# Optimization experiments

Measured on AMD Instinct MI355X. Metric: run time of the kernel, lower is better.

The kernel has to match this reference:

```python
import jax, jax.numpy as jnp
import numpy as np

EPS = 1e-6
BASE_TAU = 1.0  # temperature, learnable_tau=False


def setup_inputs() -> dict:
    key = jax.random.key(0)
    k1, k2, k3 = jax.random.split(key, 3)
    n, b, t, h = 16, 4, 2048, 1024
    num_blocks = 24
    return {
        "values": jax.random.normal(k1, (n, b, t, h), dtype=jnp.float32),
        "w_query": jax.random.normal(k2, (num_blocks, h), dtype=jnp.float32) * 0.02,
        "key_pos_bias": jax.random.normal(k3, (num_blocks, h), dtype=jnp.float32) * 0.02,
        "position": 16,
    }


def reference(values, w_query, key_pos_bias, position):
    # values: [n, b, t, h] stacked completed block outputs, n == position
    fp = values.astype(jnp.float32)
    # weight-free RMSNorm (BlockAttnRes._rms_norm)
    inv = jax.lax.rsqrt(jnp.mean(fp * fp, axis=-1, keepdims=True) + EPS)
    keys = fp * inv
    # positional bias for the first `position` block slots
    keys = keys + key_pos_bias[:position].astype(keys.dtype)[:, None, None, :]
    query = w_query[position].astype(jnp.float32)  # [h]
    scale = jnp.sqrt(jnp.float32(values.shape[-1])) * BASE_TAU
    scores = jnp.einsum('h,nbth->nbt', query, keys) / scale  # [n, b, t]
    alpha = jax.nn.softmax(scores, axis=0)                    # softmax over history n
    routed = jnp.einsum('nbt,nbth->bth', alpha, fp).astype(values.dtype)
    alpha_bth = jnp.transpose(alpha, (1, 2, 0))               # [b, t, n]
    return routed, alpha_bth
```

## Files before the change

kernel.cpp:

```cpp
#include <hip/hip_runtime.h>
#include <math.h>

#define H     1024
#define NBLK  16
#define BT    8192
#define ROUTED_SIZE (BT * H)
#define SCALE_INV (1.0f / 32.0f)

typedef float v4f __attribute__((ext_vector_type(4)));

__global__ __launch_bounds__(1024) void qb_kernel(
    const float* __restrict__ w_query,
    const float* __restrict__ key_pos_bias,
    const int*   __restrict__ pos_p,
    float*       __restrict__ qb)
{
    const int n    = threadIdx.x >> 6;
    const int lane = threadIdx.x & 63;
    const int pos  = *pos_p;

    const float* q = w_query      + (size_t)pos * H;
    const float* b = key_pos_bias + (size_t)n   * H;

    float s = 0.0f;
#pragma unroll
    for (int j = 0; j < 4; ++j) {
        const int h = lane * 16 + j * 4;
        const float4 qv = *(const float4*)(q + h);
        const float4 bv = *(const float4*)(b + h);
        s += qv.x * bv.x + qv.y * bv.y + qv.z * bv.z + qv.w * bv.w;
    }
#pragma unroll
    for (int off = 32; off; off >>= 1) s += __shfl_xor(s, off, 64);
    if (lane == 0) qb[n] = s;
}

__global__ __launch_bounds__(256, 4) void block_attn_res_kernel(
    const float* __restrict__ values,
    const float* __restrict__ w_query,
    const int*   __restrict__ pos_p,
    const float* __restrict__ qb,
    float*       __restrict__ out)
{
    const int bt  = blockIdx.x;
    const int tid = threadIdx.x;
    const int h0  = tid << 2;

    const int pos = *pos_p;
    const v4f q = *(const v4f*)(w_query + (size_t)pos * H + h0);

    v4f v[NBLK];
    const float* vbase = values + (size_t)bt * H + h0;
#pragma unroll
    for (int n = 0; n < NBLK; ++n)
        v[n] = __builtin_nontemporal_load((const v4f*)(vbase + (size_t)n * BT * H));

    __shared__ float2 pv[NBLK][256];

#pragma unroll
    for (int n = 0; n < NBLK; ++n) {
        const v4f x  = v[n];
        const v4f xx = x * x;
        const v4f qx = q * x;
        const float ss = (xx[0] + xx[1]) + (xx[2] + xx[3]);
        const float qv = (qx[0] + qx[1]) + (qx[2] + qx[3]);
        pv[n][tid] = make_float2(ss, qv);
    }
    __syncthreads();

    {
        const int n2 = tid >> 4;
        const int c  = tid & 15;
        float ss = 0.0f, qv = 0.0f;
#pragma unroll
        for (int k = 0; k < 16; ++k) {
            const float2 p = pv[n2][k * 16 + c];
            ss += p.x; qv += p.y;
        }
#pragma unroll
        for (int off = 1; off <= 8; off <<= 1) {
            ss += __shfl_xor(ss, off, 64);
            qv += __shfl_xor(qv, off, 64);
        }
        if (c == 0) {
            const float inv = rsqrtf(ss * (1.0f / (float)H) + 1e-6f);
            pv[n2][0].x = (inv * qv + qb[n2]) * SCALE_INV;
        }
    }
    __syncthreads();

    float m = -3.402823466e38f;
#pragma unroll
    for (int n = 0; n < NBLK; ++n) m = fmaxf(m, pv[n][0].x);

    float a[NBLK];
    float sum = 0.0f;
#pragma unroll
    for (int n = 0; n < NBLK; ++n) { a[n] = __expf(pv[n][0].x - m); sum += a[n]; }
    const float rs = 1.0f / sum;

    v4f acc = {0.0f, 0.0f, 0.0f, 0.0f};
#pragma unroll
    for (int n = 0; n < NBLK; ++n) acc += (a[n] * rs) * v[n];
    __builtin_nontemporal_store(acc, (v4f*)(out + (size_t)bt * H + h0));

    if (tid < NBLK)
        out[(size_t)ROUTED_SIZE + (size_t)bt * NBLK + tid]
            = __expf(pv[tid][0].x - m) * rs;
}

extern "C" void kernel_launch(void* const* d_in, const int* in_sizes, int n_in,
                              void* d_out, int out_size, void* d_ws, size_t ws_size,
                              hipStream_t stream) {
    const float* values       = (const float*)d_in[0];
    const float* w_query      = (const float*)d_in[1];
    const float* key_pos_bias = (const float*)d_in[2];
    const int*   position     = (const int*)d_in[3];
    float*       out          = (float*)d_out;
    float*       qb           = (float*)d_ws;

    hipLaunchKernelGGL(qb_kernel, dim3(1), dim3(1024), 0, stream,
                       w_query, key_pos_bias, position, qb);
    hipLaunchKernelGGL(block_attn_res_kernel, dim3(BT), dim3(256), 0, stream,
                       values, w_query, position, qb, out);
}
```

Measured before the change: 674.0 us.

## Split history dimension across four thread groups per block with 1024 threads

Each block now uses 1024 threads, with four groups of 256 each loading four of the sixteen history slices. This replaces one 256-thread block holding all sixteen vec4 loads in registers, cutting registers per thread and raising memory-level parallelism. The weighted partial sums are reduced through shared memory, and the score reduction now uses full-wavefront shuffles. The loads also change from nontemporal to ordinary loads. In exchange the block gains an extra barrier and a shared-memory round trip, and the large blocks may limit occupancy.

```diff
diff --git a/kernel.cpp b/kernel.cpp
--- a/kernel.cpp
+++ b/kernel.cpp
@@ -35,7 +35,7 @@
     if (lane == 0) qb[n] = s;
 }
 
-__global__ __launch_bounds__(256, 4) void block_attn_res_kernel(
+__global__ __launch_bounds__(1024, 8) void block_attn_res_kernel(
     const float* __restrict__ values,
     const float* __restrict__ w_query,
     const int*   __restrict__ pos_p,
@@ -44,69 +44,82 @@
 {
     const int bt  = blockIdx.x;
     const int tid = threadIdx.x;
-    const int h0  = tid << 2;
+    const int c   = tid & 255;
+    const int g   = tid >> 8;
+    const int h0  = c << 2;
+
+    __shared__ float2 pv[NBLK][256];
+    __shared__ v4f    rp[4][256];
+    __shared__ float  scores[NBLK];
 
     const int pos = *pos_p;
     const v4f q = *(const v4f*)(w_query + (size_t)pos * H + h0);
 
-    v4f v[NBLK];
-    const float* vbase = values + (size_t)bt * H + h0;
+    v4f v[4];
+    const float* vbase = values + (size_t)bt * H + h0 + (size_t)g * 4 * BT * H;
 #pragma unroll
-    for (int n = 0; n < NBLK; ++n)
-        v[n] = __builtin_nontemporal_load((const v4f*)(vbase + (size_t)n * BT * H));
-
-    __shared__ float2 pv[NBLK][256];
+    for (int i = 0; i < 4; ++i)
+        v[i] = *(const v4f*)(vbase + (size_t)i * BT * H);
 
 #pragma unroll
-    for (int n = 0; n < NBLK; ++n) {
-        const v4f x  = v[n];
+    for (int i = 0; i < 4; ++i) {
+        const v4f x  = v[i];
         const v4f xx = x * x;
         const v4f qx = q * x;
-        const float ss = (xx[0] + xx[1]) + (xx[2] + xx[3]);
-        const float qv = (qx[0] + qx[1]) + (qx[2] + qx[3]);
-        pv[n][tid] = make_float2(ss, qv);
+        pv[g * 4 + i][c] = make_float2((xx[0] + xx[1]) + (xx[2] + xx[3]),
+                                       (qx[0] + qx[1]) + (qx[2] + qx[3]));
     }
     __syncthreads();
 
     {
-        const int n2 = tid >> 4;
-        const int c  = tid & 15;
-        float ss = 0.0f, qv = 0.0f;
+        const int n2   = tid >> 6;
+        const int lane = tid & 63;
+        const float2 p0 = pv[n2][lane];
+        const float2 p1 = pv[n2][lane + 64];
+        const float2 p2 = pv[n2][lane + 128];
+        const float2 p3 = pv[n2][lane + 192];
+        float ss = (p0.x + p1.x) + (p2.x + p3.x);
+        float qv = (p0.y + p1.y) + (p2.y + p3.y);
 #pragma unroll
-        for (int k = 0; k < 16; ++k) {
-            const float2 p = pv[n2][k * 16 + c];
-            ss += p.x; qv += p.y;
-        }
-#pragma unroll
-        for (int off = 1; off <= 8; off <<= 1) {
+        for (int off = 32; off; off >>= 1) {
             ss += __shfl_xor(ss, off, 64);
             qv += __shfl_xor(qv, off, 64);
         }
-        if (c == 0) {
+        if (lane == 0) {
             const float inv = rsqrtf(ss * (1.0f / (float)H) + 1e-6f);
-            pv[n2][0].x = (inv * qv + qb[n2]) * SCALE_INV;
+            scores[n2] = (inv * qv + qb[n2]) * SCALE_INV;
         }
     }
     __syncthreads();
 
     float m = -3.402823466e38f;
 #pragma unroll
-    for (int n = 0; n < NBLK; ++n) m = fmaxf(m, pv[n][0].x);
+    for (int n = 0; n < NBLK; ++n) m = fmaxf(m, scores[n]);
 
-    float a[NBLK];
+    float ag[4];
     float sum = 0.0f;
 #pragma unroll
-    for (int n = 0; n < NBLK; ++n) { a[n] = __expf(pv[n][0].x - m); sum += a[n]; }
+    for (int n = 0; n < NBLK; ++n) {
+        const float e = __expf(scores[n] - m);
+        sum += e;
+        if ((n >> 2) == g) ag[n & 3] = e;
+    }
     const float rs = 1.0f / sum;
 
     v4f acc = {0.0f, 0.0f, 0.0f, 0.0f};
 #pragma unroll
-    for (int n = 0; n < NBLK; ++n) acc += (a[n] * rs) * v[n];
-    __builtin_nontemporal_store(acc, (v4f*)(out + (size_t)bt * H + h0));
+    for (int i = 0; i < 4; ++i) acc += (ag[i] * rs) * v[i];
+    rp[g][c] = acc;
+    __syncthreads();
+
+    if (g == 0) {
+        const v4f r = (rp[0][c] + rp[1][c]) + (rp[2][c] + rp[3][c]);
+        __builtin_nontemporal_store(r, (v4f*)(out + (size_t)bt * H + h0));
+    }
 
     if (tid < NBLK)
         out[(size_t)ROUTED_SIZE + (size_t)bt * NBLK + tid]
-            = __expf(pv[tid][0].x - m) * rs;
+            = __expf(scores[tid] - m) * rs;
 }
 
 extern "C" void kernel_launch(void* const* d_in, const int* in_sizes, int n_in,
@@ -121,6 +134,6 @@
 
     hipLaunchKernelGGL(qb_kernel, dim3(1), dim3(1024), 0, stream,
                        w_query, key_pos_bias, position, qb);
-    hipLaunchKernelGGL(block_attn_res_kernel, dim3(BT), dim3(256), 0, stream,
+    hipLaunchKernelGGL(block_attn_res_kernel, dim3(BT), dim3(1024), 0, stream,
                        values, w_query, position, qb, out);
 }
```

Result: no change. 682.8 us (+1.3%).
